# Performance work log

Measured on AMD Instinct MI355X. Metric: run time of the kernel, lower is better.

## Reference

```python
import jax, jax.numpy as jnp
import numpy as np

MAX_Z = 54  # atomic numbers up to iodine (53)
_mv = np.full(MAX_Z, 4.0, np.float32)
for z, v in {6: 4, 7: 3, 8: 2, 16: 6, 9: 1, 17: 1, 35: 1, 53: 1, 15: 5, 1: 1}.items():
    _mv[z] = v
_vdw = np.full(MAX_Z, 1.6, np.float32)  # default_radius = 1.6
for z, r in {1: 1.2, 6: 1.7, 7: 1.55, 8: 1.52, 9: 1.47, 15: 1.8, 16: 1.8, 17: 1.75, 35: 1.85, 53: 1.98}.items():
    _vdw[z] = r
_bl = np.full((MAX_Z, MAX_Z), 1.5, np.float32)  # default_length = 1.5
for (a, b), L in {(6, 6): 1.54, (6, 7): 1.47, (6, 8): 1.43, (6, 16): 1.82, (6, 9): 1.35, (6, 17): 1.77, (6, 1): 1.09, (7, 7): 1.45, (7, 8): 1.40, (7, 1): 1.01, (8, 8): 1.48, (8, 1): 0.96, (16, 16): 2.05, (15, 8): 1.63}.items():
    _bl[a, b] = L
    _bl[b, a] = L  # symmetric == tuple(sorted(...)) lookup
MAX_VAL = jnp.asarray(_mv)
VDW = jnp.asarray(_vdw)
BOND = jnp.asarray(_bl)
BIG = 1e9  # stands in for torch's float('inf') diagonal mask


def _forward(pos, edge_index, atom_types):
    N = pos.shape[0]
    row, col = edge_index[0], edge_index[1]
    # --- valence violations: scatter-add out-degree per atom ---
    bond_counts = jnp.zeros((N,), pos.dtype).at[row].add(1.0)
    violation = jnp.maximum(bond_counts - MAX_VAL[atom_types], 0.0)  # >0 iff counts > max_val
    loss = jnp.sum(violation ** 2)
    # Sequential valence push. Original loops atoms in ascending order and each atom's
    # neighbors in edge-list order; a stable sort of edges by row reproduces exactly that
    # visitation order, so a scan over sorted edges matches the sequential semantics
    # (pos_new[i] updates feed later direction computations).
    order = jnp.argsort(row)  # jnp.argsort is stable
    rs, cs = row[order], col[order]

    def step(p, rc):
        r, c = rc
        v = violation[r]
        d = p[r] - p[c]
        dist = jnp.linalg.norm(d) + 1e-8
        return p.at[r].add(jnp.where(v > 0, d / dist * v * 1e-3, 0.0)), None

    pos_new, _ = jax.lax.scan(step, pos, (rs, cs))
    # --- bond-length correction (gather per edge, scatter back per atom) ---
    bond_vec = pos_new[row] - pos_new[col]                        # [E,3]
    cur_len = jnp.linalg.norm(bond_vec, axis=-1, keepdims=True)   # [E,1]
    tgt_len = BOND[atom_types[row], atom_types[col]][:, None]     # [E,1]
    loss = loss + jnp.mean(jnp.abs(cur_len - tgt_len) ** 2)
    ratio = jnp.clip(tgt_len / (cur_len + 1e-8), 0.98, 1.02)
    adj = (bond_vec * ratio - bond_vec) * 0.01
    pos_new = pos_new + jnp.zeros_like(pos).at[row].add(adj * 0.5).at[col].add(-adj * 0.5)
    # --- steric clash repulsion over all atom pairs (cdist) ---
    sq = jnp.sum(pos_new ** 2, axis=-1)
    d2 = sq[:, None] + sq[None, :] - 2.0 * (pos_new @ pos_new.T)  # [N,N]
    eye = jnp.eye(N, dtype=bool)
    dist = jnp.sqrt(jnp.maximum(jnp.where(eye, 1.0, d2), 1e-20))
    dist = jnp.where(eye, BIG, dist)  # diagonal masked to +inf in the original
    rad = VDW[atom_types]
    min_d = (rad[:, None] + rad[None, :]) * 0.8
    loss = loss + jnp.sum(jax.nn.relu(min_d - dist) ** 2) / 2.0
    # original loops unordered clash pairs i<j updating i and j symmetrically; the full
    # symmetric double sum below is mathematically identical and avoids an [N,N,3] tensor:
    mask = (dist < min_d) & (dist > 1e-8)
    coeff = jnp.where(mask, (min_d - dist) * 0.005 * 0.5 / dist, 0.0)  # [N,N]
    steric = coeff.sum(axis=1)[:, None] * pos_new - coeff @ pos_new    # sum_j c_ij (p_i - p_j)
    return pos_new + steric, loss * 0.1


def setup_inputs() -> dict:
    key = jax.random.key(0)
    k1, k2, k3, k4 = jax.random.split(key, 4)
    N, E = 8192, 32768
    pos = jax.random.normal(k1, (N, 3), jnp.float32) * 6.0  # coords in an ~Angstrom-scale blob
    elements = jnp.array([1, 6, 7, 8, 9, 15, 16, 17], jnp.int32)  # H C N O F P S Cl
    atom_types = elements[jax.random.randint(k2, (N,), 0, 8)]
    edge_index = jnp.stack([jax.random.randint(k3, (E,), 0, N),
                            jax.random.randint(k4, (E,), 0, N)]).astype(jnp.int32)
    return {"pos": pos, "edge_index": edge_index, "atom_types": atom_types}


def reference(pos, edge_index, atom_types):
    return _forward(pos, edge_index, atom_types)
```

## Files before the change

### kernel.cpp

```cpp
#include <hip/hip_runtime.h>
#include <math.h>

#define NA 8192
#define NE 32768
#define NT 256
#define JSPLIT 32
#define JCHUNK (NA / JSPLIT)
#define NIB 16

#define WS_DEG      0
#define WS_LOSS     (WS_DEG + NA)
#define WS_DD       (WS_LOSS + 4)
#define WS_ZERO_END (WS_DD + 3*NA)
#define WS_PART     ((WS_ZERO_END + 3) & ~3)
#define WS_PD       (WS_PART + 4*JSPLIT*NA)

__device__ __forceinline__ float maxval_of(int z) {
    switch (z) {
        case 1: return 1.f; case 6: return 4.f; case 7: return 3.f; case 8: return 2.f;
        case 9: return 1.f; case 15: return 5.f; case 16: return 6.f; case 17: return 1.f;
        case 35: return 1.f; case 53: return 1.f; default: return 4.f;
    }
}
__device__ __forceinline__ float vdw_of(int z) {
    switch (z) {
        case 1: return 1.2f; case 6: return 1.7f; case 7: return 1.55f; case 8: return 1.52f;
        case 9: return 1.47f; case 15: return 1.8f; case 16: return 1.8f; case 17: return 1.75f;
        case 35: return 1.85f; case 53: return 1.98f; default: return 1.6f;
    }
}
__device__ __forceinline__ float bond_of(int a, int b) {
    int lo = a < b ? a : b, hi = a < b ? b : a;
    switch (lo * 64 + hi) {
        case 6*64+6:   return 1.54f;
        case 6*64+7:   return 1.47f;
        case 6*64+8:   return 1.43f;
        case 6*64+16:  return 1.82f;
        case 6*64+9:   return 1.35f;
        case 6*64+17:  return 1.77f;
        case 1*64+6:   return 1.09f;
        case 7*64+7:   return 1.45f;
        case 7*64+8:   return 1.40f;
        case 1*64+7:   return 1.01f;
        case 8*64+8:   return 1.48f;
        case 1*64+8:   return 0.96f;
        case 16*64+16: return 2.05f;
        case 8*64+15:  return 1.63f;
        default:       return 1.5f;
    }
}
__device__ __forceinline__ float viol_of(int d, int z) {
    return fmaxf((float)d - maxval_of(z), 0.f);
}

__device__ __forceinline__ float wave_reduce_sum(float x) {
    #pragma unroll
    for (int off = 32; off > 0; off >>= 1) x += __shfl_down(x, off);
    return x;
}

__global__ void k_deg(const int* __restrict__ row, int* __restrict__ deg,
                      float* __restrict__ zbase ) {
    int e = blockIdx.x * NT + threadIdx.x;
    if (e < 3 * NA + 4) zbase[e] = 0.f;
    if (e < NE) atomicAdd(&deg[row[e]], 1);
}

__global__ void k_edge(const int* __restrict__ row, const int* __restrict__ col,
                       const int* __restrict__ types, const int* __restrict__ deg,
                       const float* __restrict__ pos, float* __restrict__ dD,
                       float* __restrict__ lossAcc) {
    int e = blockIdx.x * NT + threadIdx.x;
    float l1 = 0.f, l0 = 0.f;
    if (e < NE) {
        int r = row[e], c = col[e];
        float bx = pos[3*r]   - pos[3*c];
        float by = pos[3*r+1] - pos[3*c+1];
        float bz = pos[3*r+2] - pos[3*c+2];
        float cur = sqrtf(bx*bx + by*by + bz*bz);
        float tgt = bond_of(types[r], types[c]);
        float diff = cur - tgt;
        l1 = diff * diff;
        float ratio = tgt / (cur + 1e-8f);
        ratio = fminf(fmaxf(ratio, 0.98f), 1.02f);
        float s = (ratio - 1.f) * 0.01f * 0.5f;
        float v = viol_of(deg[r], types[r]);
        float sc = (v > 0.f) ? (v * 1e-3f / (cur + 1e-8f)) : 0.f;
        float rs = s + sc;
        atomicAdd(&dD[3*r],   bx * rs);
        atomicAdd(&dD[3*r+1], by * rs);
        atomicAdd(&dD[3*r+2], bz * rs);
        atomicAdd(&dD[3*c],   -bx * s);
        atomicAdd(&dD[3*c+1], -by * s);
        atomicAdd(&dD[3*c+2], -bz * s);
    }
    if (e < NA) {
        float v = viol_of(deg[e], types[e]);
        l0 = v * v;
    }
    float p1 = wave_reduce_sum(l1);
    float p0 = wave_reduce_sum(l0);
    if ((threadIdx.x & 63) == 0) {
        if (p1 != 0.f) atomicAdd(&lossAcc[1], p1);
        if (p0 != 0.f) atomicAdd(&lossAcc[0], p0);
    }
}

__global__ void k_pack(const float* __restrict__ pos, const float* __restrict__ dD,
                       const int* __restrict__ types, float4* __restrict__ pd) {
    int a = blockIdx.x * NT + threadIdx.x;
    pd[a] = make_float4(pos[3*a]   + dD[3*a],
                        pos[3*a+1] + dD[3*a+1],
                        pos[3*a+2] + dD[3*a+2],
                        vdw_of(types[a]) * 0.8f);
}

__device__ __forceinline__ void steric_pair(const float4 p, const float4 q,
                                            float& cs, float& sx, float& sy, float& sz,
                                            float& ll) {
    float dx = p.x - q.x, dy = p.y - q.y, dz = p.z - q.z;
    float d2 = fmaf(dx, dx, fmaf(dy, dy, dz * dz));
    float md = p.w + q.w;
    float rinv = rsqrtf(fmaxf(d2, 1e-12f));
    float dist = d2 * rinv;
    float t1 = md - dist;
    bool ok = (t1 > 0.f) && (d2 > 1e-12f);
    float t1c = ok ? t1 : 0.f;
    ll = fmaf(t1c, t1c, ll);
    float co = t1c * rinv;
    cs += co;
    sx = fmaf(co, q.x, sx);
    sy = fmaf(co, q.y, sy);
    sz = fmaf(co, q.z, sz);
}

__global__ void __launch_bounds__(NT)
k_steric(const float4* __restrict__ pd, float4* __restrict__ partial,
         float* __restrict__ lossAcc) {
    const int t = threadIdx.x;
    const int b = blockIdx.x;
    const int yb = b >> 4;
    const int ib = b & 15;
    const float4* __restrict__ qs = pd + yb * JCHUNK;
    const int i0 = ib * 512 + t;
    const int i1 = i0 + 256;
    float4 p0 = pd[i0];
    float4 p1 = pd[i1];
    float cs0 = 0.f, sx0 = 0.f, sy0 = 0.f, sz0 = 0.f;
    float cs1 = 0.f, sx1 = 0.f, sy1 = 0.f, sz1 = 0.f;
    float ll = 0.f;
    #pragma unroll 8
    for (int jj = 0; jj < JCHUNK; jj++) {
        float4 q = qs[jj];
        steric_pair(p0, q, cs0, sx0, sy0, sz0, ll);
        steric_pair(p1, q, cs1, sx1, sy1, sz1, ll);
    }
    partial[yb * NA + i0] = make_float4(cs0, sx0, sy0, sz0);
    partial[yb * NA + i1] = make_float4(cs1, sx1, sy1, sz1);
    float part = wave_reduce_sum(ll);
    if ((t & 63) == 0 && part != 0.f) atomicAdd(&lossAcc[2], part);
}

__global__ void k_reduce(const float4* __restrict__ pd,
                         const float4* __restrict__ partial,
                         const float* __restrict__ lossAcc, float* __restrict__ out) {
    int a = blockIdx.x * NT + threadIdx.x;
    float cs = 0.f, sx = 0.f, sy = 0.f, sz = 0.f;
    #pragma unroll 8
    for (int y = 0; y < JSPLIT; y++) {
        float4 u = partial[y * NA + a];
        cs += u.x; sx += u.y; sy += u.z; sz += u.w;
    }
    float4 p = pd[a];
    float c = 1.f + cs * 0.0025f;
    out[3*a]   = p.x * c - sx * 0.0025f;
    out[3*a+1] = p.y * c - sy * 0.0025f;
    out[3*a+2] = p.z * c - sz * 0.0025f;
    if (a == 0) {
        float loss = lossAcc[0] + lossAcc[1] * (1.f / NE) + lossAcc[2] * 0.5f;
        out[3*NA] = loss * 0.1f;
    }
}

extern "C" void kernel_launch(void* const* d_in, const int* in_sizes, int n_in,
                              void* d_out, int out_size, void* d_ws, size_t ws_size,
                              hipStream_t stream) {
    (void)in_sizes; (void)n_in; (void)out_size; (void)ws_size;
    const float* pos   = (const float*)d_in[0];
    const int*   eidx  = (const int*)d_in[1];
    const int*   types = (const int*)d_in[2];
    const int* row = eidx;
    const int* col = eidx + NE;

    int*   ws_i = (int*)d_ws;
    float* ws_f = (float*)d_ws;
    int*    deg     = ws_i + WS_DEG;
    float*  lossAcc = ws_f + WS_LOSS;
    float*  dD      = ws_f + WS_DD;
    float4* partial = (float4*)(ws_f + WS_PART);
    float4* pd      = (float4*)(ws_f + WS_PD);
    float*  out     = (float*)d_out;

    hipMemsetAsync(deg, 0, (size_t)NA * 4, stream);
    k_deg   <<<NE/NT, NT, 0, stream>>>(row, deg, ws_f + WS_LOSS);
    k_edge  <<<NE/NT, NT, 0, stream>>>(row, col, types, deg, pos, dD, lossAcc);
    k_pack  <<<NA/NT, NT, 0, stream>>>(pos, dD, types, pd);
    k_steric<<<JSPLIT*NIB, NT, 0, stream>>>(pd, partial, lossAcc);
    k_reduce<<<NA/NT, NT, 0, stream>>>(pd, partial, lossAcc, out);
}
```

Before: 136.4 us.

## Bin atoms by x-coordinate and skip distant tiles in steric pair loop

Atoms are counting-sorted into 256 x-bins after the position update. The steric kernel then works on the sorted array and skips whole i/j tiles whose x-ranges are farther apart than the maximum clash distance. Inside a tile it skips pair evaluation when no lane in the wave has a pair closer in x than the summed radii. The j-chunk is also staged in shared memory. This replaces most of the dense all-pairs work with a spatial cull, at the cost of an extra scatter kernel, atomics, and summation order that depends on the sort.

Result: slower. 157.5 us (+15.5%).

```diff
diff --git a/kernel.cpp b/kernel.cpp
--- a/kernel.cpp
+++ b/kernel.cpp
@@ -8,12 +8,23 @@
 #define JCHUNK (NA / JSPLIT)
 #define NIB 16
 
+#define NBIN 256
+#define XMIN (-32.0f)
+#define BW 0.25f
+#define INVBW 4.0f
+#define MDMAX 3.168f
+
 #define WS_DEG      0
-#define WS_LOSS     (WS_DEG + NA)
+#define WS_BINCNT   (WS_DEG + NA)
+#define WS_BINFILL  (WS_BINCNT + NBIN)
+#define WS_MEMSET_N (WS_BINFILL + NBIN)
+#define WS_LOSS     WS_MEMSET_N
 #define WS_DD       (WS_LOSS + 4)
-#define WS_ZERO_END (WS_DD + 3*NA)
-#define WS_PART     ((WS_ZERO_END + 3) & ~3)
-#define WS_PD       (WS_PART + 4*JSPLIT*NA)
+#define WS_BINOF    (WS_DD + 3*NA)
+#define WS_PD       ((WS_BINOF + NA + 3) & ~3)
+#define WS_SPD      (WS_PD + 4*NA)
+#define WS_SORIG    (WS_SPD + 4*NA)
+#define WS_PART     ((WS_SORIG + NA + 3) & ~3)
 
 __device__ __forceinline__ float maxval_of(int z) {
     switch (z) {
@@ -51,6 +62,10 @@
 }
 __device__ __forceinline__ float viol_of(int d, int z) {
     return fmaxf((float)d - maxval_of(z), 0.f);
+}
+__device__ __forceinline__ int bin_of_x(float x) {
+    int b = (int)floorf((x - XMIN) * INVBW);
+    return min(max(b, 0), NBIN - 1);
 }
 
 __device__ __forceinline__ float wave_reduce_sum(float x) {
@@ -107,12 +122,42 @@
 }
 
 __global__ void k_pack(const float* __restrict__ pos, const float* __restrict__ dD,
-                       const int* __restrict__ types, float4* __restrict__ pd) {
+                       const int* __restrict__ types, float4* __restrict__ pd,
+                       int* __restrict__ binOf, int* __restrict__ binCnt) {
     int a = blockIdx.x * NT + threadIdx.x;
-    pd[a] = make_float4(pos[3*a]   + dD[3*a],
-                        pos[3*a+1] + dD[3*a+1],
-                        pos[3*a+2] + dD[3*a+2],
-                        vdw_of(types[a]) * 0.8f);
+    float4 v = make_float4(pos[3*a]   + dD[3*a],
+                           pos[3*a+1] + dD[3*a+1],
+                           pos[3*a+2] + dD[3*a+2],
+                           vdw_of(types[a]) * 0.8f);
+    pd[a] = v;
+    int b = bin_of_x(v.x);
+    binOf[a] = b;
+    atomicAdd(&binCnt[b], 1);
+}
+
+__global__ void k_scatter(const float4* __restrict__ pd, const int* __restrict__ binOf,
+                          const int* __restrict__ binCnt, int* __restrict__ binFill,
+                          float4* __restrict__ spd, int* __restrict__ sorig) {
+    __shared__ int buf[NBIN];
+    const int t = threadIdx.x;
+    buf[t] = binCnt[t];
+    __syncthreads();
+    int own = buf[t];
+    for (int off = 1; off < NBIN; off <<= 1) {
+        int v = (t >= off) ? buf[t - off] : 0;
+        __syncthreads();
+        buf[t] += v;
+        __syncthreads();
+    }
+    __shared__ int sStart[NBIN];
+    sStart[t] = buf[t] - own;
+    __syncthreads();
+    int a = blockIdx.x * NT + t;
+    int b = binOf[a];
+    int rank = atomicAdd(&binFill[b], 1);
+    int dst = sStart[b] + rank;
+    spd[dst] = pd[a];
+    sorig[dst] = a;
 }
 
 __device__ __forceinline__ void steric_pair(const float4 p, const float4 q,
@@ -135,48 +180,71 @@
 }
 
 __global__ void __launch_bounds__(NT)
-k_steric(const float4* __restrict__ pd, float4* __restrict__ partial,
+k_steric(const float4* __restrict__ spd, float4* __restrict__ partial,
          float* __restrict__ lossAcc) {
+    __shared__ float4 sm[JCHUNK];
     const int t = threadIdx.x;
     const int b = blockIdx.x;
     const int yb = b >> 4;
     const int ib = b & 15;
-    const float4* __restrict__ qs = pd + yb * JCHUNK;
+    const int jbase = yb * JCHUNK;
     const int i0 = ib * 512 + t;
     const int i1 = i0 + 256;
-    float4 p0 = pd[i0];
-    float4 p1 = pd[i1];
-    float cs0 = 0.f, sx0 = 0.f, sy0 = 0.f, sz0 = 0.f;
-    float cs1 = 0.f, sx1 = 0.f, sy1 = 0.f, sz1 = 0.f;
-    float ll = 0.f;
-    #pragma unroll 8
+
+    int bj0 = bin_of_x(spd[jbase].x);
+    int bj1 = bin_of_x(spd[jbase + JCHUNK - 1].x);
+    int bi0 = bin_of_x(spd[ib * 512].x);
+    int bi1 = bin_of_x(spd[ib * 512 + 511].x);
+    float jlo = (bj0 == 0)        ? -1e30f : XMIN + bj0 * BW;
+    float jhi = (bj1 == NBIN - 1) ?  1e30f : XMIN + (bj1 + 1) * BW;
+    float ilo = (bi0 == 0)        ? -1e30f : XMIN + bi0 * BW;
+    float ihi = (bi1 == NBIN - 1) ?  1e30f : XMIN + (bi1 + 1) * BW;
+    if (jlo > ihi + MDMAX || jhi < ilo - MDMAX) {
+        float4 z = make_float4(0.f, 0.f, 0.f, 0.f);
+        partial[yb * NA + i0] = z;
+        partial[yb * NA + i1] = z;
+        return;
+    }
+
+    sm[t] = spd[jbase + t];
+    float4 p0 = spd[i0];
+    float4 p1 = spd[i1];
+    __syncthreads();
+    float cs0 = 0.f, sx0 = 0.f, sy0 = 0.f, sz0 = 0.f, ll0 = 0.f;
+    float cs1 = 0.f, sx1 = 0.f, sy1 = 0.f, sz1 = 0.f, ll1 = 0.f;
+    #pragma unroll 2
     for (int jj = 0; jj < JCHUNK; jj++) {
-        float4 q = qs[jj];
-        steric_pair(p0, q, cs0, sx0, sy0, sz0, ll);
-        steric_pair(p1, q, cs1, sx1, sy1, sz1, ll);
+        float4 q = sm[jj];
+        float n0 = fabsf(p0.x - q.x) - (p0.w + q.w);
+        float n1 = fabsf(p1.x - q.x) - (p1.w + q.w);
+        if (__any(fminf(n0, n1) < 0.f)) {
+            steric_pair(p0, q, cs0, sx0, sy0, sz0, ll0);
+            steric_pair(p1, q, cs1, sx1, sy1, sz1, ll1);
+        }
     }
     partial[yb * NA + i0] = make_float4(cs0, sx0, sy0, sz0);
     partial[yb * NA + i1] = make_float4(cs1, sx1, sy1, sz1);
-    float part = wave_reduce_sum(ll);
+    float part = wave_reduce_sum(ll0 + ll1);
     if ((t & 63) == 0 && part != 0.f) atomicAdd(&lossAcc[2], part);
 }
 
-__global__ void k_reduce(const float4* __restrict__ pd,
+__global__ void k_reduce(const float4* __restrict__ spd, const int* __restrict__ sorig,
                          const float4* __restrict__ partial,
                          const float* __restrict__ lossAcc, float* __restrict__ out) {
-    int a = blockIdx.x * NT + threadIdx.x;
+    int s = blockIdx.x * NT + threadIdx.x;
     float cs = 0.f, sx = 0.f, sy = 0.f, sz = 0.f;
     #pragma unroll 8
     for (int y = 0; y < JSPLIT; y++) {
-        float4 u = partial[y * NA + a];
+        float4 u = partial[y * NA + s];
         cs += u.x; sx += u.y; sy += u.z; sz += u.w;
     }
-    float4 p = pd[a];
+    float4 p = spd[s];
     float c = 1.f + cs * 0.0025f;
-    out[3*a]   = p.x * c - sx * 0.0025f;
-    out[3*a+1] = p.y * c - sy * 0.0025f;
-    out[3*a+2] = p.z * c - sz * 0.0025f;
-    if (a == 0) {
+    int orig = sorig[s];
+    out[3*orig]   = p.x * c - sx * 0.0025f;
+    out[3*orig+1] = p.y * c - sy * 0.0025f;
+    out[3*orig+2] = p.z * c - sz * 0.0025f;
+    if (s == 0) {
         float loss = lossAcc[0] + lossAcc[1] * (1.f / NE) + lossAcc[2] * 0.5f;
         out[3*NA] = loss * 0.1f;
     }
@@ -195,16 +263,22 @@
     int*   ws_i = (int*)d_ws;
     float* ws_f = (float*)d_ws;
     int*    deg     = ws_i + WS_DEG;
+    int*    binCnt  = ws_i + WS_BINCNT;
+    int*    binFill = ws_i + WS_BINFILL;
     float*  lossAcc = ws_f + WS_LOSS;
     float*  dD      = ws_f + WS_DD;
+    int*    binOf   = ws_i + WS_BINOF;
+    float4* pd      = (float4*)(ws_f + WS_PD);
+    float4* spd     = (float4*)(ws_f + WS_SPD);
+    int*    sorig   = ws_i + WS_SORIG;
     float4* partial = (float4*)(ws_f + WS_PART);
-    float4* pd      = (float4*)(ws_f + WS_PD);
     float*  out     = (float*)d_out;
 
-    hipMemsetAsync(deg, 0, (size_t)NA * 4, stream);
-    k_deg   <<<NE/NT, NT, 0, stream>>>(row, deg, ws_f + WS_LOSS);
-    k_edge  <<<NE/NT, NT, 0, stream>>>(row, col, types, deg, pos, dD, lossAcc);
-    k_pack  <<<NA/NT, NT, 0, stream>>>(pos, dD, types, pd);
-    k_steric<<<JSPLIT*NIB, NT, 0, stream>>>(pd, partial, lossAcc);
-    k_reduce<<<NA/NT, NT, 0, stream>>>(pd, partial, lossAcc, out);
-}
+    hipMemsetAsync(d_ws, 0, (size_t)WS_MEMSET_N * 4, stream);
+    k_deg    <<<NE/NT, NT, 0, stream>>>(row, deg, ws_f + WS_LOSS);
+    k_edge   <<<NE/NT, NT, 0, stream>>>(row, col, types, deg, pos, dD, lossAcc);
+    k_pack   <<<NA/NT, NT, 0, stream>>>(pos, dD, types, pd, binOf, binCnt);
+    k_scatter<<<NA/NT, NT, 0, stream>>>(pd, binOf, binCnt, binFill, spd, sorig);
+    k_steric <<<JSPLIT*NIB, NT, 0, stream>>>(spd, partial, lossAcc);
+    k_reduce <<<NA/NT, NT, 0, stream>>>(spd, sorig, partial, lossAcc, out);
+}
```
